# Optimization experiments

Hardware: AMD Instinct MI355X
Metric: run time of the kernel (lower is better)

Reference implementation:

```python
import jax, jax.numpy as jnp
import numpy as np

N_EXPERTS = 64
LN_EPS = 1e-5


def _layer_norm(x, gamma, beta, eps=LN_EPS):
    mu = jnp.mean(x, axis=-1, keepdims=True)
    var = jnp.mean(jnp.square(x - mu), axis=-1, keepdims=True)
    return (x - mu) * jax.lax.rsqrt(var + eps) * gamma + beta


def setup_inputs() -> dict:
    key = jax.random.key(0)
    ks = jax.random.split(key, 4)
    B, T, D, Ff = 2, 1024, 512, 2048
    x = jax.random.normal(ks[0], (B, T, D), dtype=jnp.float32)
    hex_weights = jax.random.uniform(ks[1], (B, T, N_EXPERTS), dtype=jnp.float32)
    W_in = jax.random.normal(ks[2], (N_EXPERTS, Ff, D), dtype=jnp.float32) * (D ** -0.5)
    b_in = jnp.zeros((N_EXPERTS, Ff), dtype=jnp.float32)
    W_out = jax.random.normal(ks[3], (N_EXPERTS, D, Ff), dtype=jnp.float32) * (Ff ** -0.5)
    b_out = jnp.zeros((N_EXPERTS, D), dtype=jnp.float32)
    ln_gamma = jnp.ones((D,), dtype=jnp.float32)
    ln_beta = jnp.zeros((D,), dtype=jnp.float32)
    return {"x": x, "hex_weights": hex_weights, "W_in": W_in, "b_in": b_in,
            "W_out": W_out, "b_out": b_out, "ln_gamma": ln_gamma,
            "ln_beta": ln_beta, "top_k": 4}


def reference(x, hex_weights, W_in, b_in, W_out, b_out, ln_gamma, ln_beta, top_k):
    B, T, D = x.shape
    N = B * T
    x_n = _layer_norm(x, ln_gamma, ln_beta)

    # top-k routing; renormalize the selected weights (matches torch topk + sum-norm)
    top_w, top_idx = jax.lax.top_k(hex_weights, top_k)          # (B,T,k)
    top_w = top_w / (jnp.sum(top_w, axis=-1, keepdims=True) + 1e-8)

    x_flat = x_n.reshape(N, D)
    # Scatter the k normalized weights into a dense (N, 64) routing matrix.
    # Non-selected experts get weight 0, so a dense per-expert sweep computes
    # EXACTLY the same combined output as the per-token gather in the original.
    w_full = jnp.zeros((N, N_EXPERTS), dtype=x.dtype)
    w_full = w_full.at[jnp.arange(N)[:, None], top_idx.reshape(N, top_k)].set(
        top_w.reshape(N, top_k))

    def body(acc, e):
        W_in_e, b_in_e, W_out_e, b_out_e, we = e  # we: (N,)
        h = jax.nn.silu(x_flat @ W_in_e.T + b_in_e)            # (N, d_ff)
        acc = acc + we[:, None] * (h @ W_out_e.T + b_out_e)    # (N, D)
        return acc, None

    acc, _ = jax.lax.scan(body, jnp.zeros_like(x_flat),
                          (W_in, b_in, W_out, b_out, w_full.T))
    return acc.reshape(B, T, D)
```

## Files before the change

kernel.cpp:

```cpp
#include <hip/hip_runtime.h>

#define NTOK 2048
#define DD   512
#define FFD  2048
#define NE   64
#define KSEL 4
#define NPAIR (NTOK*KSEL)
#define BM 192
#define BK 64
#define NT 128
#define HROWS (NPAIR + 256)

typedef short s16x8 __attribute__((ext_vector_type(8)));
typedef float f32x4 __attribute__((ext_vector_type(4)));

typedef const __attribute__((address_space(1))) char* gptr_t;
typedef __attribute__((address_space(3))) char* lptr_t;

static __device__ __forceinline__ unsigned short f2bf(float f) {
    unsigned int u = __builtin_bit_cast(unsigned int, f);
    u += 0x7FFFu + ((u >> 16) & 1u);
    return (unsigned short)(u >> 16);
}

static __device__ __forceinline__ void packwrite(char* base, int nn, int kb, float4 v) {
    unsigned int lo = (unsigned int)f2bf(v.x) | ((unsigned int)f2bf(v.y) << 16);
    unsigned int hi = (unsigned int)f2bf(v.z) | ((unsigned int)f2bf(v.w) << 16);
    *(uint2*)(base + nn * 128 + (kb ^ ((nn & 7) << 4))) = make_uint2(lo, hi);
}

__global__ __launch_bounds__(256) void k_ln_route(
    const float* __restrict__ x, const float* __restrict__ hw,
    const float* __restrict__ gamma, const float* __restrict__ beta,
    unsigned short* __restrict__ xn_bf, int* __restrict__ counts,
    int* __restrict__ tok_e, float* __restrict__ tok_w)
{
    const int t = blockIdx.x;
    const int tid = threadIdx.x;
    const float* xr = x + (size_t)t * DD;
    float v0 = xr[tid];
    float v1 = xr[tid + 256];
    float s = v0 + v1, s2 = v0*v0 + v1*v1;
    #pragma unroll
    for (int off = 32; off > 0; off >>= 1) {
        s  += __shfl_down(s, off);
        s2 += __shfl_down(s2, off);
    }
    __shared__ float rsum[4], rsum2[4];
    __shared__ float smu, srs;
    const int wid = tid >> 6, lane = tid & 63;
    if (lane == 0) { rsum[wid] = s; rsum2[wid] = s2; }
    __syncthreads();
    if (tid == 0) {
        float a = 0.f, b = 0.f;
        for (int i = 0; i < 4; ++i) { a += rsum[i]; b += rsum2[i]; }
        float mu  = a * (1.f / DD);
        float var = b * (1.f / DD) - mu * mu;
        smu = mu; srs = rsqrtf(var + 1e-5f);
    }
    __syncthreads();
    const float mu = smu, rstd = srs;
    xn_bf[(size_t)t*DD + tid]       = f2bf((v0 - mu) * rstd * gamma[tid]       + beta[tid]);
    xn_bf[(size_t)t*DD + tid + 256] = f2bf((v1 - mu) * rstd * gamma[tid + 256] + beta[tid + 256]);

    if (tid < 64) {
        float v = hw[(size_t)t*NE + tid];
        int   sel[KSEL]; float sw[KSEL];
        #pragma unroll
        for (int j = 0; j < KSEL; ++j) {
            float m = v; int mi = tid;
            #pragma unroll
            for (int off = 32; off > 0; off >>= 1) {
                float ov = __shfl_xor(m, off);
                int   oi = __shfl_xor(mi, off);
                if (ov > m || (ov == m && oi < mi)) { m = ov; mi = oi; }
            }
            if (tid == mi) v = -1e30f;
            sel[j] = mi; sw[j] = m;
        }
        if (tid == 0) {
            float ssum = sw[0] + sw[1] + sw[2] + sw[3];
            float inv = 1.f / (ssum + 1e-8f);
            #pragma unroll
            for (int j = 0; j < KSEL; ++j) {
                tok_e[t*KSEL + j] = sel[j];
                tok_w[t*KSEL + j] = sw[j] * inv;
                atomicAdd(&counts[sel[j]], 1);
            }
        }
    }
}

__global__ void k_scan(const int* __restrict__ counts, int* __restrict__ offs,
                       int* __restrict__ cursor, int* __restrict__ tile_e,
                       int* __restrict__ tile_r, int* __restrict__ ntiles)
{
    __shared__ int sc[NE], stc[NE];
    const int tid = threadIdx.x;
    sc[tid] = counts[tid];
    __syncthreads();
    int off = 0;
    for (int i = 0; i < tid; ++i) off += sc[i];
    offs[tid] = off; cursor[tid] = off;
    if (tid == NE-1) offs[NE] = off + sc[NE-1];
    int tc = (sc[tid] + BM - 1) / BM;
    stc[tid] = tc;
    __syncthreads();
    int toff = 0;
    for (int i = 0; i < tid; ++i) toff += stc[i];
    for (int j = 0; j < tc; ++j) { tile_e[toff + j] = tid; tile_r[toff + j] = off + j*BM; }
    if (tid == NE-1) *ntiles = toff + tc;
}

__global__ __launch_bounds__(256) void k_scatter(
    const int* __restrict__ tok_e, const float* __restrict__ tok_w,
    int* __restrict__ cursor, int* __restrict__ pair_tok,
    float* __restrict__ pair_w, int* __restrict__ inv)
{
    int i = blockIdx.x * 256 + threadIdx.x;
    if (i >= NPAIR) return;
    int t = i >> 2;
    int e = tok_e[i];
    int slot = atomicAdd(&cursor[e], 1);
    pair_tok[slot] = t;
    pair_w[slot] = tok_w[i];
    inv[i] = slot;
}

template<int KD, bool IS_IN, int BNX, int NYG>
__global__ __launch_bounds__(256, 2) void k_moe_gemm(
    const unsigned short* __restrict__ Abf,
    const float* __restrict__ W, const float* __restrict__ bias,
    const int* __restrict__ tile_e, const int* __restrict__ tile_r,
    const int* __restrict__ ntiles, const int* __restrict__ offs,
    const int* __restrict__ pr_tok, const float* __restrict__ pr_w,
    unsigned short* __restrict__ Hout, float* __restrict__ Pout)
{
    constexpr int NK = KD / BK;
    constexpr int NB = BNX / 16;
    constexpr int MT = IS_IN ? 6 : 3;
    const int ti = ((blockIdx.x >> 3) / NYG) * 8 + (blockIdx.x & 7);
    const int yg = (blockIdx.x >> 3) & (NYG - 1);
    if (ti >= *ntiles) return;
    const int e    = tile_e[ti];
    const int row0 = tile_r[ti];
    const int rend = offs[e + 1];
    const int n0   = yg * BNX;
    const int NOUT = IS_IN ? FFD : DD;
    const float* __restrict__ Wb = W + (size_t)e * NOUT * KD;

    __shared__ __align__(16) unsigned short As[2 * BM * BK];
    __shared__ __align__(16) unsigned short Bs[2 * BNX * BK];

    const int tid  = threadIdx.x;
    const int lane = tid & 63, wave = tid >> 6;
    const int wmbase = IS_IN ? (wave >> 1) * 96 : wave * 48;
    const int wnbase = IS_IN ? (wave & 1) * 64 : 0;

    const char* asrc[6];
    #pragma unroll
    for (int i = 0; i < 6; ++i) {
        int seg  = wave * 6 + i;
        int r    = seg * 8 + (lane >> 3);
        int grow = row0 + r;
        int cg   = (lane & 7) ^ (r & 7);
        size_t rowbase;
        if (IS_IN) {
            int tok = (grow < rend) ? pr_tok[grow] : pr_tok[row0];
            rowbase = (size_t)tok * (KD * 2);
        } else {
            rowbase = (size_t)grow * (KD * 2);
        }
        asrc[i] = (const char*)Abf + rowbase + (size_t)cg * 16;
    }

    const float* wsrc0 = Wb + (size_t)(n0 + (tid >> 4)) * KD + (tid & 15) * 4;
    const int nb = tid >> 4;
    const int kb = (tid & 15) * 8;

    f32x4 acc[MT][4];
    #pragma unroll
    for (int m = 0; m < MT; ++m)
        #pragma unroll
        for (int n = 0; n < 4; ++n)
            acc[m][n] = (f32x4){0.f, 0.f, 0.f, 0.f};

    {
        #pragma unroll
        for (int i = 0; i < 6; ++i)
            __builtin_amdgcn_global_load_lds((gptr_t)asrc[i],
                (lptr_t)((char*)As + (wave * 6 + i) * 1024), 16, 0, 0);
        float4 breg[NB];
        #pragma unroll
        for (int i = 0; i < NB; ++i)
            breg[i] = *(const float4*)(wsrc0 + (size_t)i * 16 * KD);
        #pragma unroll
        for (int i = 0; i < NB; ++i)
            packwrite((char*)Bs, nb + i * 16, kb, breg[i]);
    }
    __syncthreads();

    int buf = 0;
    for (int kt = 0; kt < NK; ++kt) {
        const int k0n = (kt + 1) * BK;
        float4 bregN[NB];
        if (kt + 1 < NK) {
            #pragma unroll
            for (int i = 0; i < 6; ++i)
                __builtin_amdgcn_global_load_lds((gptr_t)(asrc[i] + (size_t)k0n * 2),
                    (lptr_t)((char*)As + (buf ^ 1) * (BM * BK * 2) + (wave * 6 + i) * 1024),
                    16, 0, 0);
            #pragma unroll
            for (int i = 0; i < NB; ++i)
                bregN[i] = *(const float4*)(wsrc0 + (size_t)i * 16 * KD + k0n);
        }
        __builtin_amdgcn_sched_barrier(0);

        const char* Ab = (const char*)As + buf * (BM * BK * 2);
        const char* Bb = (const char*)Bs + buf * (BNX * BK * 2);
        #pragma unroll
        for (int h = 0; h < 2; ++h) {
            s16x8 af[MT], bfr[4];
            const int koff = h * 64 + (lane >> 4) * 16;
            #pragma unroll
            for (int m = 0; m < MT; ++m) {
                int row = wmbase + m * 16 + (lane & 15);
                af[m] = *(const s16x8*)(Ab + row * 128 + (koff ^ ((row & 7) << 4)));
            }
            #pragma unroll
            for (int n = 0; n < 4; ++n) {
                int row = wnbase + n * 16 + (lane & 15);
                bfr[n] = *(const s16x8*)(Bb + row * 128 + (koff ^ ((row & 7) << 4)));
            }
            #pragma unroll
            for (int m = 0; m < MT; ++m)
                #pragma unroll
                for (int n = 0; n < 4; ++n)
                    acc[m][n] = __builtin_amdgcn_mfma_f32_16x16x32_bf16(af[m], bfr[n], acc[m][n], 0, 0, 0);
        }
        __builtin_amdgcn_sched_barrier(0);

        if (kt + 1 < NK) {
            char* Bw = (char*)Bs + (buf ^ 1) * (BNX * BK * 2);
            #pragma unroll
            for (int i = 0; i < NB; ++i)
                packwrite(Bw, nb + i * 16, kb, bregN[i]);
        }
        __syncthreads();
        buf ^= 1;
    }

    #pragma unroll
    for (int m = 0; m < MT; ++m) {
        #pragma unroll
        for (int r = 0; r < 4; ++r) {
            int row = row0 + wmbase + m * 16 + (lane >> 4) * 4 + r;
            if (row < rend) {
                if (IS_IN) {
                    #pragma unroll
                    for (int n = 0; n < 4; ++n) {
                        int f = n0 + wnbase + n * 16 + (lane & 15);
                        float v = acc[m][n][r] + bias[e * FFD + f];
                        v = v / (1.f + __expf(-v));
                        Hout[(size_t)row * FFD + f] = f2bf(v);
                    }
                } else {
                    float pw = pr_w[row];
                    #pragma unroll
                    for (int n = 0; n < 4; ++n) {
                        int d = n0 + wnbase + n * 16 + (lane & 15);
                        Pout[(size_t)row * DD + d] = (acc[m][n][r] + bias[e * DD + d]) * pw;
                    }
                }
            }
        }
    }
}

__global__ __launch_bounds__(128) void k_combine(
    const float* __restrict__ pout, const int* __restrict__ inv,
    float* __restrict__ out)
{
    const int t = blockIdx.x;
    const int tid = threadIdx.x;
    const float4* p0 = (const float4*)(pout + (size_t)inv[t*4+0]*DD);
    const float4* p1 = (const float4*)(pout + (size_t)inv[t*4+1]*DD);
    const float4* p2 = (const float4*)(pout + (size_t)inv[t*4+2]*DD);
    const float4* p3 = (const float4*)(pout + (size_t)inv[t*4+3]*DD);
    float4 a = p0[tid], b = p1[tid], c = p2[tid], d = p3[tid];
    float4 r;
    r.x = a.x + b.x + c.x + d.x;
    r.y = a.y + b.y + c.y + d.y;
    r.z = a.z + b.z + c.z + d.z;
    r.w = a.w + b.w + c.w + d.w;
    ((float4*)(out + (size_t)t*DD))[tid] = r;
}

extern "C" void kernel_launch(void* const* d_in, const int* in_sizes, int n_in,
                              void* d_out, int out_size, void* d_ws, size_t ws_size,
                              hipStream_t stream)
{
    const float* x     = (const float*)d_in[0];
    const float* hw    = (const float*)d_in[1];
    const float* Win   = (const float*)d_in[2];
    const float* bin   = (const float*)d_in[3];
    const float* Wout  = (const float*)d_in[4];
    const float* bout  = (const float*)d_in[5];
    const float* gamma = (const float*)d_in[6];
    const float* beta  = (const float*)d_in[7];
    float* out = (float*)d_out;

    char* ws = (char*)d_ws;
    size_t o = 0;
    unsigned short* xn_bf = (unsigned short*)(ws + o); o += (size_t)NTOK * DD * 2;
    unsigned short* H     = (unsigned short*)(ws + o); o += (size_t)HROWS * FFD * 2;
    float* pout   = (float*)(ws + o); o += (size_t)NPAIR * DD * 4;
    int*   counts = (int*)(ws + o);   o += 256;
    int*   offs   = (int*)(ws + o);   o += 512;
    int*   cursor = (int*)(ws + o);   o += 256;
    int*   tok_e  = (int*)(ws + o);   o += (size_t)NPAIR * 4;
    float* tok_w  = (float*)(ws + o); o += (size_t)NPAIR * 4;
    int*   inv    = (int*)(ws + o);   o += (size_t)NPAIR * 4;
    int*   pr_tok = (int*)(ws + o);   o += (size_t)NPAIR * 4;
    float* pr_w   = (float*)(ws + o); o += (size_t)NPAIR * 4;
    int*   tile_e = (int*)(ws + o);   o += 512;
    int*   tile_r = (int*)(ws + o);   o += 512;
    int*   ntiles = (int*)(ws + o);   o += 256;
    (void)ws_size; (void)in_sizes; (void)n_in; (void)out_size;

    hipMemsetAsync(counts, 0, 256, stream);
    k_ln_route<<<dim3(NTOK), dim3(256), 0, stream>>>(x, hw, gamma, beta, xn_bf, counts, tok_e, tok_w);
    k_scan<<<dim3(1), dim3(64), 0, stream>>>(counts, offs, cursor, tile_e, tile_r, ntiles);
    k_scatter<<<dim3(NPAIR/256), dim3(256), 0, stream>>>(tok_e, tok_w, cursor, pr_tok, pr_w, inv);

    k_moe_gemm<DD, true, 128, FFD/128><<<dim3(NT * (FFD/128)), dim3(256), 0, stream>>>(
        xn_bf, Win, bin, tile_e, tile_r, ntiles, offs, pr_tok, pr_w, H, nullptr);
    k_moe_gemm<FFD, false, 64, DD/64><<<dim3(NT * (DD/64)), dim3(256), 0, stream>>>(
        H, Wout, bout, tile_e, tile_r, ntiles, offs, pr_tok, pr_w, nullptr, pout);

    k_combine<<<dim3(NTOK), dim3(128), 0, stream>>>(pout, inv, out);
}
```

Baseline: 231.4 us.

## Fuse scan with scatter and combine via atomicAdd in down-projection epilogue

Merges the prefix-scan and pair-scatter kernels into one single-block kernel. It also drops the per-pair output buffer and the combine kernel: the second GEMM now atomically adds weighted results straight into the zeroed output. This removes two launches and a 16 MB intermediate write and read. The cost is scalar float atomics to global memory, a serialized scatter inside a single workgroup, and a non-deterministic summation order.

```diff
diff --git a/kernel.cpp b/kernel.cpp
--- a/kernel.cpp
+++ b/kernel.cpp
@@ -91,40 +91,37 @@
     }
 }
 
-__global__ void k_scan(const int* __restrict__ counts, int* __restrict__ offs,
-                       int* __restrict__ cursor, int* __restrict__ tile_e,
-                       int* __restrict__ tile_r, int* __restrict__ ntiles)
+__global__ __launch_bounds__(256) void k_scan_scatter(
+    const int* __restrict__ counts, int* __restrict__ offs,
+    int* __restrict__ cursor, int* __restrict__ tile_e,
+    int* __restrict__ tile_r, int* __restrict__ ntiles,
+    const int* __restrict__ tok_e, const float* __restrict__ tok_w,
+    int* __restrict__ pair_tok, float* __restrict__ pair_w)
 {
     __shared__ int sc[NE], stc[NE];
     const int tid = threadIdx.x;
-    sc[tid] = counts[tid];
-    __syncthreads();
-    int off = 0;
-    for (int i = 0; i < tid; ++i) off += sc[i];
-    offs[tid] = off; cursor[tid] = off;
-    if (tid == NE-1) offs[NE] = off + sc[NE-1];
-    int tc = (sc[tid] + BM - 1) / BM;
-    stc[tid] = tc;
-    __syncthreads();
-    int toff = 0;
-    for (int i = 0; i < tid; ++i) toff += stc[i];
-    for (int j = 0; j < tc; ++j) { tile_e[toff + j] = tid; tile_r[toff + j] = off + j*BM; }
-    if (tid == NE-1) *ntiles = toff + tc;
-}
-
-__global__ __launch_bounds__(256) void k_scatter(
-    const int* __restrict__ tok_e, const float* __restrict__ tok_w,
-    int* __restrict__ cursor, int* __restrict__ pair_tok,
-    float* __restrict__ pair_w, int* __restrict__ inv)
-{
-    int i = blockIdx.x * 256 + threadIdx.x;
-    if (i >= NPAIR) return;
-    int t = i >> 2;
-    int e = tok_e[i];
-    int slot = atomicAdd(&cursor[e], 1);
-    pair_tok[slot] = t;
-    pair_w[slot] = tok_w[i];
-    inv[i] = slot;
+    if (tid < NE) sc[tid] = counts[tid];
+    __syncthreads();
+    if (tid < NE) {
+        int off = 0;
+        for (int i = 0; i < tid; ++i) off += sc[i];
+        offs[tid] = off; cursor[tid] = off;
+        if (tid == NE-1) offs[NE] = off + sc[NE-1];
+        int tc = (sc[tid] + BM - 1) / BM;
+        stc[tid] = tc;
+        __builtin_amdgcn_s_barrier();
+        int toff = 0;
+        for (int i = 0; i < tid; ++i) toff += stc[i];
+        for (int j = 0; j < tc; ++j) { tile_e[toff + j] = tid; tile_r[toff + j] = off + j*BM; }
+        if (tid == NE-1) *ntiles = toff + tc;
+    }
+    __syncthreads();
+    for (int i = tid; i < NPAIR; i += 256) {
+        int e = tok_e[i];
+        int slot = atomicAdd(&cursor[e], 1);
+        pair_tok[slot] = i >> 2;
+        pair_w[slot]  = tok_w[i];
+    }
 }
 
 template<int KD, bool IS_IN, int BNX, int NYG>
@@ -134,13 +131,13 @@
     const int* __restrict__ tile_e, const int* __restrict__ tile_r,
     const int* __restrict__ ntiles, const int* __restrict__ offs,
     const int* __restrict__ pr_tok, const float* __restrict__ pr_w,
-    unsigned short* __restrict__ Hout, float* __restrict__ Pout)
+    unsigned short* __restrict__ Hout, float* __restrict__ Out)
 {
     constexpr int NK = KD / BK;
     constexpr int NB = BNX / 16;
     constexpr int MT = IS_IN ? 6 : 3;
     const int ti = ((blockIdx.x >> 3) / NYG) * 8 + (blockIdx.x & 7);
-    const int yg = (blockIdx.x >> 3) & (NYG - 1);
+    const int yg = (blockIdx.x >> 3) % NYG;
     if (ti >= *ntiles) return;
     const int e    = tile_e[ti];
     const int row0 = tile_r[ti];
@@ -265,35 +262,17 @@
                         Hout[(size_t)row * FFD + f] = f2bf(v);
                     }
                 } else {
-                    float pw = pr_w[row];
+                    float pw  = pr_w[row];
+                    int   tok = pr_tok[row];
                     #pragma unroll
                     for (int n = 0; n < 4; ++n) {
                         int d = n0 + wnbase + n * 16 + (lane & 15);
-                        Pout[(size_t)row * DD + d] = (acc[m][n][r] + bias[e * DD + d]) * pw;
+                        atomicAdd(&Out[(size_t)tok * DD + d], (acc[m][n][r] + bias[e * DD + d]) * pw);
                     }
                 }
             }
         }
     }
-}
-
-__global__ __launch_bounds__(128) void k_combine(
-    const float* __restrict__ pout, const int* __restrict__ inv,
-    float* __restrict__ out)
-{
-    const int t = blockIdx.x;
-    const int tid = threadIdx.x;
-    const float4* p0 = (const float4*)(pout + (size_t)inv[t*4+0]*DD);
-    const float4* p1 = (const float4*)(pout + (size_t)inv[t*4+1]*DD);
-    const float4* p2 = (const float4*)(pout + (size_t)inv[t*4+2]*DD);
-    const float4* p3 = (const float4*)(pout + (size_t)inv[t*4+3]*DD);
-    float4 a = p0[tid], b = p1[tid], c = p2[tid], d = p3[tid];
-    float4 r;
-    r.x = a.x + b.x + c.x + d.x;
-    r.y = a.y + b.y + c.y + d.y;
-    r.z = a.z + b.z + c.z + d.z;
-    r.w = a.w + b.w + c.w + d.w;
-    ((float4*)(out + (size_t)t*DD))[tid] = r;
 }
 
 extern "C" void kernel_launch(void* const* d_in, const int* in_sizes, int n_in,
@@ -314,13 +293,11 @@
     size_t o = 0;
     unsigned short* xn_bf = (unsigned short*)(ws + o); o += (size_t)NTOK * DD * 2;
     unsigned short* H     = (unsigned short*)(ws + o); o += (size_t)HROWS * FFD * 2;
-    float* pout   = (float*)(ws + o); o += (size_t)NPAIR * DD * 4;
     int*   counts = (int*)(ws + o);   o += 256;
     int*   offs   = (int*)(ws + o);   o += 512;
     int*   cursor = (int*)(ws + o);   o += 256;
     int*   tok_e  = (int*)(ws + o);   o += (size_t)NPAIR * 4;
     float* tok_w  = (float*)(ws + o); o += (size_t)NPAIR * 4;
-    int*   inv    = (int*)(ws + o);   o += (size_t)NPAIR * 4;
     int*   pr_tok = (int*)(ws + o);   o += (size_t)NPAIR * 4;
     float* pr_w   = (float*)(ws + o); o += (size_t)NPAIR * 4;
     int*   tile_e = (int*)(ws + o);   o += 512;
@@ -329,14 +306,13 @@
     (void)ws_size; (void)in_sizes; (void)n_in; (void)out_size;
 
     hipMemsetAsync(counts, 0, 256, stream);
+    hipMemsetAsync(out, 0, (size_t)NTOK * DD * 4, stream);
     k_ln_route<<<dim3(NTOK), dim3(256), 0, stream>>>(x, hw, gamma, beta, xn_bf, counts, tok_e, tok_w);
-    k_scan<<<dim3(1), dim3(64), 0, stream>>>(counts, offs, cursor, tile_e, tile_r, ntiles);
-    k_scatter<<<dim3(NPAIR/256), dim3(256), 0, stream>>>(tok_e, tok_w, cursor, pr_tok, pr_w, inv);
+    k_scan_scatter<<<dim3(1), dim3(256), 0, stream>>>(counts, offs, cursor, tile_e, tile_r,
+                                                      ntiles, tok_e, tok_w, pr_tok, pr_w);
 
     k_moe_gemm<DD, true, 128, FFD/128><<<dim3(NT * (FFD/128)), dim3(256), 0, stream>>>(
         xn_bf, Win, bin, tile_e, tile_r, ntiles, offs, pr_tok, pr_w, H, nullptr);
     k_moe_gemm<FFD, false, 64, DD/64><<<dim3(NT * (DD/64)), dim3(256), 0, stream>>>(
-        H, Wout, bout, tile_e, tile_r, ntiles, offs, pr_tok, pr_w, nullptr, pout);
-
-    k_combine<<<dim3(NTOK), dim3(128), 0, stream>>>(pout, inv, out);
-}
+        H, Wout, bout, tile_e, tile_r, ntiles, offs, pr_tok, pr_w, nullptr, out);
+}
```

Measured after the change: 277.7 us. +20.0%, slower.
